# Performance work log

Measured on AMD Instinct MI355X. Metric: run time of the kernel, lower is better.

The kernel has to match this reference:

```python
import jax, jax.numpy as jnp
import numpy as np
import math

B, S, D = 4, 2048, 1024
N_HEADS = 16
D_FF = 4096
T_DIM = 256
KEEP_RATIO = 0.7
EPS = 1e-5


def _layernorm(x):
    mu = jnp.mean(x, axis=-1, keepdims=True)
    var = jnp.mean((x - mu) ** 2, axis=-1, keepdims=True)
    return (x - mu) * jax.lax.rsqrt(var + EPS)


def _ada_ln(x, cond, W, b):
    # cond: (B, T_DIM); W: (2D, T_DIM)
    p = jax.nn.silu(cond) @ W.T + b            # (B, 2D)
    gamma, beta = jnp.split(p, 2, axis=-1)
    return _layernorm(x) * (1.0 + gamma[:, None, :]) + beta[:, None, :]


def _mha(h, in_w, in_b, out_w, out_b):
    b, s, d = h.shape
    hd = d // N_HEADS
    qkv = h @ in_w.T + in_b                     # (b, s, 3d)
    q, k, v = jnp.split(qkv, 3, axis=-1)
    def heads(t):
        return t.reshape(b, s, N_HEADS, hd).transpose(0, 2, 1, 3)
    q, k, v = heads(q), heads(k), heads(v)
    scores = jnp.einsum('bhqd,bhkd->bhqk', q, k) / math.sqrt(hd)
    attn = jax.nn.softmax(scores, axis=-1)
    o = jnp.einsum('bhqk,bhkd->bhqd', attn, v)  # (b, h, s, hd)
    o = o.transpose(0, 2, 1, 3).reshape(b, s, d)
    return o @ out_w.T + out_b


def setup_inputs() -> dict:
    key = jax.random.key(0)
    ks = jax.random.split(key, 24)
    sc = 0.02
    return {
        'x': jax.random.normal(ks[0], (B, S, D), jnp.float32),
        't_emb': jax.random.normal(ks[1], (B, T_DIM), jnp.float32),
        'tr_w1': jax.random.normal(ks[2], (32, D), jnp.float32) * sc,
        'tr_b1': jnp.zeros((32,), jnp.float32),
        'tr_w2': jax.random.normal(ks[3], (1, 32), jnp.float32) * sc,
        'tr_b2': jnp.zeros((1,), jnp.float32),
        'ln1_w': jax.random.normal(ks[4], (2 * D, T_DIM), jnp.float32) * sc,
        'ln1_b': jnp.zeros((2 * D,), jnp.float32),
        'ln2_w': jax.random.normal(ks[5], (2 * D, T_DIM), jnp.float32) * sc,
        'ln2_b': jnp.zeros((2 * D,), jnp.float32),
        'in_proj_w': jax.random.normal(ks[6], (3 * D, D), jnp.float32) * sc,
        'in_proj_b': jnp.zeros((3 * D,), jnp.float32),
        'out_w': jax.random.normal(ks[7], (D, D), jnp.float32) * sc,
        'out_b': jnp.zeros((D,), jnp.float32),
        'ffn_w1': jax.random.normal(ks[8], (D_FF, D), jnp.float32) * sc,
        'ffn_b1': jnp.zeros((D_FF,), jnp.float32),
        'ffn_w2': jax.random.normal(ks[9], (D, D_FF), jnp.float32) * sc,
        'ffn_b2': jnp.zeros((D,), jnp.float32),
        # torch inits gates to zero; use small randn so the block is non-trivial
        'gate_attn': jax.random.normal(ks[10], (1, 1, D), jnp.float32) * sc,
        'gate_ffn': jax.random.normal(ks[11], (1, 1, D), jnp.float32) * sc,
    }


def reference(x, t_emb, tr_w1, tr_b1, tr_w2, tr_b2, ln1_w, ln1_b, ln2_w, ln2_b,
              in_proj_w, in_proj_b, out_w, out_b, ffn_w1, ffn_b1, ffn_w2, ffn_b2,
              gate_attn, gate_ffn):
    b, s, d = x.shape
    num_keep = max(int(s * KEEP_RATIO), 1)

    # token importance on detached x (stop_gradient mirrors x.detach())
    xd = jax.lax.stop_gradient(x)
    imp = jax.nn.silu(xd @ tr_w1.T + tr_b1) @ tr_w2.T + tr_b2  # (b, s, 1)
    imp = imp[..., 0]
    _, idx = jax.lax.top_k(imp, num_keep)
    idx = jnp.sort(idx, axis=-1)                               # (b, num_keep)

    x_sel = jnp.take_along_axis(x, idx[..., None], axis=1)     # (b, k, d)

    h = _ada_ln(x_sel, t_emb, ln1_w, ln1_b)
    h = _mha(h, in_proj_w, in_proj_b, out_w, out_b)
    x_sel = x_sel + gate_attn * h

    h = _ada_ln(x_sel, t_emb, ln2_w, ln2_b)
    h = jax.nn.gelu(h @ ffn_w1.T + ffn_b1, approximate=False) @ ffn_w2.T + ffn_b2
    x_sel = x_sel + gate_ffn * h

    batch_idx = jnp.arange(b)[:, None]
    return x.at[batch_idx, idx].set(x_sel)
```

## Files before the change

### kernel.cpp

```cpp
#include <hip/hip_runtime.h>
#include <hip/hip_bf16.h>
#include <cmath>
#include <cstdint>

typedef __bf16 bf16;
typedef __bf16 bf16x8 __attribute__((ext_vector_type(8)));
typedef __bf16 bf16x4 __attribute__((ext_vector_type(4)));
typedef float  f32x4  __attribute__((ext_vector_type(4)));

constexpr int B_   = 4;
constexpr int S_   = 2048;
constexpr int D_   = 1024;
constexpr int H_   = 16;
constexpr int DFF_ = 4096;
constexpr int TD_  = 256;
constexpr int KEEP = 1433;
constexpr int M_TOT = B_ * KEEP;
constexpr int MPAD  = 5760;
constexpr int QT64  = (KEEP + 63) / 64;
constexpr int NKV   = (KEEP + 63) / 64;
constexpr float EPS = 1e-5f;
constexpr float QSCALE = 0.18033688011112042f;

__device__ __forceinline__ f32x4 mfma16(bf16x8 a, bf16x8 b, f32x4 c) {
  return __builtin_amdgcn_mfma_f32_16x16x32_bf16(a, b, c, 0, 0, 0);
}

#define GLOAD_LDS(gp, lp)                                                     \
  __builtin_amdgcn_global_load_lds(                                           \
      (const __attribute__((address_space(1))) void*)(gp),                    \
      (__attribute__((address_space(3))) void*)(lp), 16, 0, 0)

__global__ __launch_bounds__(256) void k_impgemv(
    const float* __restrict__ x, const float* __restrict__ w1,
    double* __restrict__ hidden)
{
  const int lane = threadIdx.x & 63, w = threadIdx.x >> 6;
  const int tok0 = blockIdx.x * 16 + w * 4;
  const int u0 = blockIdx.y * 8;
  const float* xb = x + (size_t)tok0 * D_ + lane * 4;
  const float* wb = w1 + (size_t)u0 * D_ + lane * 4;
  double acc[4][8] = {};
#pragma unroll 2
  for (int c = 0; c < D_; c += 256) {
    float4 xv[4], wv[8];
#pragma unroll
    for (int i = 0; i < 4; ++i)
      xv[i] = *(const float4*)(xb + (size_t)i * D_ + c);
#pragma unroll
    for (int u = 0; u < 8; ++u)
      wv[u] = *(const float4*)(wb + (size_t)u * D_ + c);
#pragma unroll
    for (int i = 0; i < 4; ++i)
#pragma unroll
      for (int u = 0; u < 8; ++u) {
        acc[i][u] += (double)xv[i].x * (double)wv[u].x;
        acc[i][u] += (double)xv[i].y * (double)wv[u].y;
        acc[i][u] += (double)xv[i].z * (double)wv[u].z;
        acc[i][u] += (double)xv[i].w * (double)wv[u].w;
      }
  }
#pragma unroll
  for (int i = 0; i < 4; ++i)
#pragma unroll
    for (int u = 0; u < 8; ++u) {
      double s = acc[i][u];
      for (int o = 32; o > 0; o >>= 1) s += __shfl_xor(s, o);
      acc[i][u] = s;
    }
  if (lane == 0) {
#pragma unroll
    for (int i = 0; i < 4; ++i)
#pragma unroll
      for (int u = 0; u < 8; ++u)
        hidden[(size_t)(tok0 + i) * 32 + u0 + u] = acc[i][u];
  }
}

__global__ __launch_bounds__(256) void k_imptail(
    const double* __restrict__ hidden, const float* __restrict__ b1,
    const float* __restrict__ w2, const float* __restrict__ b2,
    double* __restrict__ imp)
{
  const int tok = blockIdx.x * 256 + threadIdx.x;
  const double* hp = hidden + (size_t)tok * 32;
  double r = 0.0;
#pragma unroll
  for (int u = 0; u < 32; ++u) {
    double s = hp[u] + (double)b1[u];
    double sv = s / (1.0 + exp(-s));
    r += sv * (double)w2[u];
  }
  imp[tok] = r + (double)b2[0];
}

__global__ __launch_bounds__(256) void k_rank(const double* __restrict__ imp,
                                              int* __restrict__ rank)
{
  const int b = blockIdx.x >> 5;
  const int seg = blockIdx.x & 31;
  __shared__ double vals[S_];
  const double* ib = imp + (size_t)b * S_;
  for (int i = threadIdx.x; i < S_ / 2; i += 256)
    ((double2*)vals)[i] = ((const double2*)ib)[i];
  __syncthreads();
  const int tl = threadIdx.x >> 2;
  const int part = threadIdx.x & 3;
  const int s = seg * 64 + tl;
  const double v = vals[s];
  int cnt = 0;
  for (int j = part * 512; j < (part + 1) * 512; ++j) {
    double u = vals[j];
    cnt += (u > v) || (u == v && j < s);
  }
  cnt += __shfl_xor(cnt, 1);
  cnt += __shfl_xor(cnt, 2);
  if (part == 0) rank[b * S_ + s] = cnt;
}

__global__ __launch_bounds__(256) void k_compact(const int* __restrict__ rank,
                                                 int* __restrict__ idx)
{
  const int b = blockIdx.x;
  __shared__ int wcnt[4];
  __shared__ int base_s;
  if (threadIdx.x == 0) base_s = 0;
  __syncthreads();
  const int t = threadIdx.x, lane = t & 63, w = t >> 6;
  for (int c = 0; c < S_ / 256; ++c) {
    const int s = c * 256 + t;
    const bool kept = rank[b * S_ + s] < KEEP;
    unsigned long long m = __ballot(kept);
    int piw = __popcll(m & ((1ull << lane) - 1ull));
    if (lane == 0) wcnt[w] = __popcll(m);
    __syncthreads();
    int off = base_s;
    for (int i = 0; i < w; ++i) off += wcnt[i];
    if (kept) idx[b * KEEP + off + piw] = s;
    __syncthreads();
    if (t == 0) base_s += wcnt[0] + wcnt[1] + wcnt[2] + wcnt[3];
    __syncthreads();
  }
}

__global__ __launch_bounds__(256) void k_condproj(
    const float* __restrict__ temb, const float* __restrict__ W,
    const float* __restrict__ bias, float* __restrict__ p)
{
  const int gw = (int)((blockIdx.x * 256 + threadIdx.x) >> 6);
  const int lane = threadIdx.x & 63;
  const int b = gw >> 11;
  const int row = gw & 2047;
  const float* te = temb + (size_t)b * TD_;
  const float* wr = W + (size_t)row * TD_;
  float acc = 0.f;
  for (int i = lane; i < TD_; i += 64) {
    float c = te[i];
    acc += (c / (1.f + __expf(-c))) * wr[i];
  }
  for (int o = 32; o > 0; o >>= 1) acc += __shfl_down(acc, o);
  if (lane == 0) p[(size_t)b * 2 * D_ + row] = acc + bias[row];
}

__global__ void k_f2b(const float* __restrict__ src, bf16* __restrict__ dst, int n4)
{
  int i = blockIdx.x * 256 + threadIdx.x;
  if (i < n4) {
    float4 v = ((const float4*)src)[i];
    bf16x4 o = {(bf16)v.x, (bf16)v.y, (bf16)v.z, (bf16)v.w};
    ((bf16x4*)dst)[i] = o;
  }
}

__global__ __launch_bounds__(256) void k_adaln(
    const float* __restrict__ xsrc, const int* __restrict__ idx,
    const float* __restrict__ p, bf16* __restrict__ hout)
{
  const int r = blockIdx.x, t = threadIdx.x;
  bf16* orow = hout + (size_t)r * D_;
  if (r >= M_TOT) {
    bf16x4 z = {(bf16)0.f, (bf16)0.f, (bf16)0.f, (bf16)0.f};
    ((bf16x4*)orow)[t] = z;
    return;
  }
  const int b = r / KEEP, j = r - b * KEEP;
  const int s = idx[b * KEEP + j];
  const float* xr = xsrc + ((size_t)(b * S_ + s)) * D_;
  float4 v = ((const float4*)xr)[t];
  __shared__ float red[8];
  float sum = v.x + v.y + v.z + v.w;
  for (int o = 32; o > 0; o >>= 1) sum += __shfl_down(sum, o);
  const int lane = t & 63, w = t >> 6;
  if (lane == 0) red[w] = sum;
  __syncthreads();
  const float mu = (red[0] + red[1] + red[2] + red[3]) * (1.f / D_);
  const float dx = v.x - mu, dy = v.y - mu, dz = v.z - mu, dw = v.w - mu;
  float vs = dx * dx + dy * dy + dz * dz + dw * dw;
  for (int o = 32; o > 0; o >>= 1) vs += __shfl_down(vs, o);
  if (lane == 0) red[4 + w] = vs;
  __syncthreads();
  const float rstd = rsqrtf((red[4] + red[5] + red[6] + red[7]) * (1.f / D_) + EPS);
  const float* gp = p + (size_t)b * 2 * D_;
  float4 g  = ((const float4*)gp)[t];
  float4 be = ((const float4*)(gp + D_))[t];
  bf16x4 o;
  o[0] = (bf16)(dx * rstd * (1.f + g.x) + be.x);
  o[1] = (bf16)(dy * rstd * (1.f + g.y) + be.y);
  o[2] = (bf16)(dz * rstd * (1.f + g.z) + be.z);
  o[3] = (bf16)(dw * rstd * (1.f + g.w) + be.w);
  ((bf16x4*)orow)[t] = o;
}

template <int BN, int MODE>
__global__ __launch_bounds__(256) void k_gemm(
    const bf16* __restrict__ A, const bf16* __restrict__ W,
    const float* __restrict__ bias, bf16* __restrict__ Cbf,
    const float* __restrict__ gate, const int* __restrict__ idx,
    float* __restrict__ resid, int N, int K, int gn)
{
  constexpr int WN = BN / 2;
  constexpr int NJ = WN / 16;
  __shared__ bf16 As[2][128 * 64];
  __shared__ bf16 Ws[2][BN * 64];
  const int t = threadIdx.x, lane = t & 63;
  const int w = t >> 6, wr = w >> 1, wc = w & 1;
  const int fr = lane & 15, fq = lane >> 4;

  const int nwg = gridDim.x, orig = blockIdx.x;
  const int q8 = nwg >> 3, r8 = nwg & 7;
  const int xc = orig & 7, pos = orig >> 3;
  const int wgid = (xc < r8 ? xc * (q8 + 1) : r8 * (q8 + 1) + (xc - r8) * q8) + pos;
  const int bm = wgid / gn, bn = wgid - bm * gn;

  const bf16* Ab = A + (size_t)bm * 128 * K;
  const bf16* Wb = W + (size_t)bn * BN * K;

  auto stage = [&](int buf, int kt) {
    const int ko = kt * 64;
#pragma unroll
    for (int it = 0; it < 4; ++it) {
      const int e = it * 256 + t;
      const int row = e >> 3, pc = e & 7;
      const int lc = pc ^ (row & 7);
      GLOAD_LDS(Ab + (size_t)row * K + ko + lc * 8, &As[buf][0] + e * 8);
    }
#pragma unroll
    for (int it = 0; it < BN / 32; ++it) {
      const int e = it * 256 + t;
      const int row = e >> 3, pc = e & 7;
      const int lc = pc ^ (row & 7);
      GLOAD_LDS(Wb + (size_t)row * K + ko + lc * 8, &Ws[buf][0] + e * 8);
    }
  };

  f32x4 acc[4][NJ] = {};
  stage(0, 0);
  const int nkt = K >> 6;
  int cur = 0;
  for (int kt = 0; kt < nkt; ++kt) {
    __syncthreads();
    if (kt + 1 < nkt) stage(cur ^ 1, kt + 1);
    const char* Al = (const char*)&As[cur][0];
    const char* Wl = (const char*)&Ws[cur][0];
#pragma unroll
    for (int kk = 0; kk < 2; ++kk) {
      bf16x8 af[4], wf[NJ];
#pragma unroll
      for (int i = 0; i < 4; ++i)
        af[i] = *(const bf16x8*)(Al + (wr * 64 + i * 16 + fr) * 128 +
                                 (((kk * 4 + fq) ^ (fr & 7)) << 4));
#pragma unroll
      for (int j = 0; j < NJ; ++j)
        wf[j] = *(const bf16x8*)(Wl + (wc * WN + j * 16 + fr) * 128 +
                                 (((kk * 4 + fq) ^ (fr & 7)) << 4));
#pragma unroll
      for (int i = 0; i < 4; ++i)
#pragma unroll
        for (int j = 0; j < NJ; ++j)
          acc[i][j] = mfma16(af[i], wf[j], acc[i][j]);
    }
    cur ^= 1;
  }

#pragma unroll
  for (int i = 0; i < 4; ++i) {
#pragma unroll
    for (int j = 0; j < NJ; ++j) {
#pragma unroll
      for (int r = 0; r < 4; ++r) {
        const int m = bm * 128 + wr * 64 + i * 16 + fq * 4 + r;
        const int n = bn * BN + wc * WN + j * 16 + fr;
        float v = acc[i][j][r] + bias[n];
        if (MODE == 0) {
          if (n < D_) v *= QSCALE;
          Cbf[(size_t)m * N + n] = (bf16)v;
        } else if (MODE == 1) {
          float gl = 0.5f * v * (1.f + erff(v * 0.70710678118654752f));
          Cbf[(size_t)m * N + n] = (bf16)gl;
        } else {
          if (m < M_TOT) {
            const int b = m / KEEP, jj = m - b * KEEP;
            const int s = idx[b * KEEP + jj];
            resid[((size_t)(b * S_ + s)) * D_ + n] += gate[n] * v;
          }
        }
      }
    }
  }
}

__global__ __launch_bounds__(256) void k_attn(const bf16* __restrict__ qkv,
                                              bf16* __restrict__ out)
{
  __shared__ bf16 Klds[2][64 * 64];
  __shared__ bf16 Vlds[2][64 * 64];

  const int t = threadIdx.x;
  const int lane = t & 63, w = t >> 6;
  const int fr = lane & 15, fq = lane >> 4;
  const int qt = blockIdx.x, h = blockIdx.y, b = blockIdx.z;
  const size_t rowbase = (size_t)b * KEEP;
  const size_t RS = 3 * D_;
  const bf16* kbase = qkv + rowbase * RS + D_ + h * 64;
  const bf16* vbase = qkv + rowbase * RS + 2 * D_ + h * 64;

  const int wq0 = qt * 64 + w * 16;
  const int qrow = min(wq0 + fr, KEEP - 1);
  const bf16* qp = qkv + (rowbase + qrow) * RS + h * 64 + fq * 8;
  const bf16x8 qf0 = *(const bf16x8*)qp;
  const bf16x8 qf1 = *(const bf16x8*)(qp + 32);

  f32x4 o[4] = {};
  float mrow = -INFINITY, lrow = 0.f;

  auto stage = [&](int buf, int kv) {
#pragma unroll
    for (int rnd = 0; rnd < 2; ++rnd) {
      const int p = rnd * 256 + t;
      {
        const int row = p >> 3, c8p = p & 7;
        const int c8 = c8p ^ ((row & 7) ^ (row >> 3));
        const int gr = min(kv + row, KEEP - 1);
        GLOAD_LDS(kbase + (size_t)gr * RS + c8 * 8, &Klds[buf][0] + p * 8);
      }
      {
        const int db = p >> 7, ksub = (p >> 3) & 15, jr = (p >> 1) & 3,
                  c8lo = p & 1;
        const int vrow = ksub * 4 + jr, vc8 = db * 2 + c8lo;
        const int gr = min(kv + vrow, KEEP - 1);
        GLOAD_LDS(vbase + (size_t)gr * RS + vc8 * 8, &Vlds[buf][0] + p * 8);
      }
    }
  };

  stage(0, 0);
  int cur = 0;

  const unsigned vbase_lds0 =
      (unsigned)(size_t)(__attribute__((address_space(3))) bf16*)&Vlds[0][0];
  const unsigned vbase_lds1 =
      (unsigned)(size_t)(__attribute__((address_space(3))) bf16*)&Vlds[1][0];

  for (int ti = 0; ti < NKV; ++ti) {
    const int kv = ti * 64;
    __syncthreads();
    if (ti + 1 < NKV) stage(cur ^ 1, kv + 64);

    const char* Kl = (const char*)&Klds[cur][0];

    f32x4 sc[4];
#pragma unroll
    for (int f = 0; f < 4; ++f) {
      const int row = ((f >> 1) << 5) + ((fr >> 2) << 3) + ((f & 1) << 1) +
                      (fr & 1) + (((fr >> 1) & 1) << 2);
      const int swz = (row & 7) ^ (row >> 3);
      const bf16x8 kf0 = *(const bf16x8*)(Kl + row * 128 + ((fq ^ swz) << 4));
      const bf16x8 kf1 =
          *(const bf16x8*)(Kl + row * 128 + (((fq ^ 4) ^ swz) << 4));
      f32x4 s = {0.f, 0.f, 0.f, 0.f};
      s = mfma16(kf0, qf0, s);
      s = mfma16(kf1, qf1, s);
      sc[f] = s;
    }

    if (ti == NKV - 1) {
#pragma unroll
      for (int f = 0; f < 4; ++f)
#pragma unroll
        for (int r = 0; r < 4; ++r) {
          const int kl = ((f >> 1) << 5) + (fq << 3) + ((f & 1) << 1) +
                         (r & 1) + ((r >> 1) << 2);
          if (kv + kl >= KEEP) sc[f][r] = -INFINITY;
        }
    }
    float mx = sc[0][0];
#pragma unroll
    for (int f = 0; f < 4; ++f)
#pragma unroll
      for (int r = 0; r < 4; ++r) mx = fmaxf(mx, sc[f][r]);
    mx = fmaxf(mx, __shfl_xor(mx, 16));
    mx = fmaxf(mx, __shfl_xor(mx, 32));
    const float mnew = fmaxf(mrow, mx);
    float ps = 0.f;
    bf16 pe[4][4];
#pragma unroll
    for (int f = 0; f < 4; ++f)
#pragma unroll
      for (int r = 0; r < 4; ++r) {
        const float pv = exp2f(sc[f][r] - mnew);
        ps += pv;
        pe[f][r] = (bf16)pv;
      }
    ps += __shfl_xor(ps, 16);
    ps += __shfl_xor(ps, 32);
    const float fac = exp2f(mrow - mnew);
    lrow = lrow * fac + ps;
    mrow = mnew;
#pragma unroll
    for (int db = 0; db < 4; ++db) {
      o[db][0] *= fac; o[db][1] *= fac; o[db][2] *= fac; o[db][3] *= fac;
    }

    const bf16x8 pb[2] = {
        {pe[0][0], pe[0][1], pe[1][0], pe[1][1],
         pe[0][2], pe[0][3], pe[1][2], pe[1][3]},
        {pe[2][0], pe[2][1], pe[3][0], pe[3][1],
         pe[2][2], pe[2][3], pe[3][2], pe[3][3]}};
    const unsigned vb =
        (cur ? vbase_lds1 : vbase_lds0) + ((unsigned)fq << 7);
#pragma unroll
    for (int c = 0; c < 2; ++c) {
      const unsigned addr = vb + c * 1024;
      bf16x4 t0, t1, t2, t3, t4, t5, t6, t7;
      asm volatile(
          "ds_read_b64_tr_b16 %0, %8 offset:0\n\t"
          "ds_read_b64_tr_b16 %1, %8 offset:128\n\t"
          "ds_read_b64_tr_b16 %2, %8 offset:2048\n\t"
          "ds_read_b64_tr_b16 %3, %8 offset:2176\n\t"
          "ds_read_b64_tr_b16 %4, %8 offset:4096\n\t"
          "ds_read_b64_tr_b16 %5, %8 offset:4224\n\t"
          "ds_read_b64_tr_b16 %6, %8 offset:6144\n\t"
          "ds_read_b64_tr_b16 %7, %8 offset:6272\n\t"
          "s_waitcnt lgkmcnt(0)"
          : "=&v"(t0), "=&v"(t1), "=&v"(t2), "=&v"(t3),
            "=&v"(t4), "=&v"(t5), "=&v"(t6), "=&v"(t7)
          : "v"(addr));
      const bf16x8 vf0 = __builtin_shufflevector(t0, t1, 0, 1, 2, 3, 4, 5, 6, 7);
      const bf16x8 vf1 = __builtin_shufflevector(t2, t3, 0, 1, 2, 3, 4, 5, 6, 7);
      const bf16x8 vf2 = __builtin_shufflevector(t4, t5, 0, 1, 2, 3, 4, 5, 6, 7);
      const bf16x8 vf3 = __builtin_shufflevector(t6, t7, 0, 1, 2, 3, 4, 5, 6, 7);
      o[0] = mfma16(vf0, pb[c], o[0]);
      o[1] = mfma16(vf1, pb[c], o[1]);
      o[2] = mfma16(vf2, pb[c], o[2]);
      o[3] = mfma16(vf3, pb[c], o[3]);
    }
    cur ^= 1;
  }

  const int q = wq0 + fr;
  if (q < KEEP) {
    const float inv = 1.f / lrow;
#pragma unroll
    for (int db = 0; db < 4; ++db) {
      bf16x4 wv = {(bf16)(o[db][0] * inv), (bf16)(o[db][1] * inv),
                   (bf16)(o[db][2] * inv), (bf16)(o[db][3] * inv)};
      *(bf16x4*)(out + (rowbase + q) * (size_t)D_ + h * 64 + db * 16 + fq * 4) =
          wv;
    }
  }
}

extern "C" void kernel_launch(void* const* d_in, const int* in_sizes, int n_in,
                              void* d_out, int out_size, void* d_ws, size_t ws_size,
                              hipStream_t stream)
{
  (void)in_sizes; (void)n_in; (void)out_size; (void)ws_size;
  const float* x      = (const float*)d_in[0];
  const float* t_emb  = (const float*)d_in[1];
  const float* tr_w1  = (const float*)d_in[2];
  const float* tr_b1  = (const float*)d_in[3];
  const float* tr_w2  = (const float*)d_in[4];
  const float* tr_b2  = (const float*)d_in[5];
  const float* ln1_w  = (const float*)d_in[6];
  const float* ln1_b  = (const float*)d_in[7];
  const float* ln2_w  = (const float*)d_in[8];
  const float* ln2_b  = (const float*)d_in[9];
  const float* in_w   = (const float*)d_in[10];
  const float* in_b   = (const float*)d_in[11];
  const float* out_w  = (const float*)d_in[12];
  const float* out_b  = (const float*)d_in[13];
  const float* f1_w   = (const float*)d_in[14];
  const float* f1_b   = (const float*)d_in[15];
  const float* f2_w   = (const float*)d_in[16];
  const float* f2_b   = (const float*)d_in[17];
  const float* gate_a = (const float*)d_in[18];
  const float* gate_f = (const float*)d_in[19];

  char* ws = (char*)d_ws;
  size_t off = 0;
  auto alloc = [&](size_t bytes) -> char* {
    char* p = ws + off;
    off = (off + bytes + 255) & ~(size_t)255;
    return p;
  };
  double* imp  = (double*)alloc((size_t)B_ * S_ * 8);
  double* hid  = (double*)alloc((size_t)B_ * S_ * 32 * 8);
  int* rank    = (int*)alloc((size_t)B_ * S_ * 4);
  int* idx     = (int*)alloc((size_t)B_ * KEEP * 4);
  float* p1    = (float*)alloc((size_t)B_ * 2 * D_ * 4);
  float* p2    = (float*)alloc((size_t)B_ * 2 * D_ * 4);
  bf16* w_in   = (bf16*)alloc((size_t)3 * D_ * D_ * 2);
  bf16* w_out  = (bf16*)alloc((size_t)D_ * D_ * 2);
  bf16* w_f1   = (bf16*)alloc((size_t)DFF_ * D_ * 2);
  bf16* w_f2   = (bf16*)alloc((size_t)D_ * DFF_ * 2);
  bf16* h_bf   = (bf16*)alloc((size_t)MPAD * D_ * 2);
  bf16* big    = (bf16*)alloc((size_t)MPAD * (3 * D_ + D_) * 2);
  bf16* qkv    = big;
  bf16* attn   = big + (size_t)MPAD * 3 * D_;
  bf16* ffn1   = big;

  hipMemcpyAsync(d_out, x, (size_t)B_ * S_ * D_ * 4, hipMemcpyDeviceToDevice, stream);

  k_impgemv<<<dim3(B_ * S_ / 16, 4), 256, 0, stream>>>(x, tr_w1, hid);
  k_imptail<<<B_ * S_ / 256, 256, 0, stream>>>(hid, tr_b1, tr_w2, tr_b2, imp);
  k_rank<<<B_ * 32, 256, 0, stream>>>(imp, rank);
  k_compact<<<B_, 256, 0, stream>>>(rank, idx);

  k_condproj<<<(B_ * 2 * D_) / 4, 256, 0, stream>>>(t_emb, ln1_w, ln1_b, p1);
  k_condproj<<<(B_ * 2 * D_) / 4, 256, 0, stream>>>(t_emb, ln2_w, ln2_b, p2);

  k_f2b<<<(3 * D_ * D_ / 4 + 255) / 256, 256, 0, stream>>>(in_w, w_in, 3 * D_ * D_ / 4);
  k_f2b<<<(D_ * D_ / 4 + 255) / 256, 256, 0, stream>>>(out_w, w_out, D_ * D_ / 4);
  k_f2b<<<(DFF_ * D_ / 4 + 255) / 256, 256, 0, stream>>>(f1_w, w_f1, DFF_ * D_ / 4);
  k_f2b<<<(DFF_ * D_ / 4 + 255) / 256, 256, 0, stream>>>(f2_w, w_f2, DFF_ * D_ / 4);

  k_adaln<<<MPAD, 256, 0, stream>>>(x, idx, p1, h_bf);
  k_gemm<128, 0><<<45 * 24, 256, 0, stream>>>(
      h_bf, w_in, in_b, qkv, nullptr, nullptr, nullptr, 3 * D_, D_, 24);
  k_attn<<<dim3(QT64, H_, B_), 256, 0, stream>>>(qkv, attn);
  k_gemm<64, 2><<<45 * 16, 256, 0, stream>>>(
      attn, w_out, out_b, nullptr, gate_a, idx, (float*)d_out, D_, D_, 16);
  k_adaln<<<MPAD, 256, 0, stream>>>((const float*)d_out, idx, p2, h_bf);
  k_gemm<128, 1><<<45 * 32, 256, 0, stream>>>(
      h_bf, w_f1, f1_b, ffn1, nullptr, nullptr, nullptr, DFF_, D_, 32);
  k_gemm<64, 2><<<45 * 16, 256, 0, stream>>>(
      ffn1, w_f2, f2_b, nullptr, gate_f, idx, (float*)d_out, D_, DFF_, 16);
}
```

Measured before the change: 457.8 us.

## Add 256x256 tile GEMM for QKV/FFN1 and streamline attention pipeline

Adds a new 512-thread GEMM kernel with 256x256 tiles, double-buffered direct-to-LDS loads, explicit vmcnt waits and an XCD-aware block remap. It is used for the QKV and FFN1 projections to raise operand reuse and cut global traffic per FLOP. M is padded to 5888 so that it divides by 256, and the other GEMM grids are adjusted to match. The attention kernel precomputes streaming K/V pointers, raises wave priority around the MFMAs, and skips the online-softmax rescale when the running max grows by less than a threshold. The larger tiles use much more LDS and registers per block, which lowers occupancy, and the lazy rescale carries a small numerical risk.

```diff
diff --git a/kernel.cpp b/kernel.cpp
--- a/kernel.cpp
+++ b/kernel.cpp
@@ -16,7 +16,7 @@
 constexpr int TD_  = 256;
 constexpr int KEEP = 1433;
 constexpr int M_TOT = B_ * KEEP;
-constexpr int MPAD  = 5760;
+constexpr int MPAD  = 5888;
 constexpr int QT64  = (KEEP + 63) / 64;
 constexpr int NKV   = (KEEP + 63) / 64;
 constexpr float EPS = 1e-5f;
@@ -30,6 +30,13 @@
   __builtin_amdgcn_global_load_lds(                                           \
       (const __attribute__((address_space(1))) void*)(gp),                    \
       (__attribute__((address_space(3))) void*)(lp), 16, 0, 0)
+
+#define FENCE_BARRIER()                                                       \
+  do {                                                                        \
+    __builtin_amdgcn_sched_barrier(0);                                        \
+    __builtin_amdgcn_s_barrier();                                             \
+    __builtin_amdgcn_sched_barrier(0);                                        \
+  } while (0)
 
 __global__ __launch_bounds__(256) void k_impgemv(
     const float* __restrict__ x, const float* __restrict__ w1,
@@ -309,6 +316,110 @@
   }
 }
 
+template <int MODE>
+__global__ __launch_bounds__(512) void k_gemm256(
+    const bf16* __restrict__ A, const bf16* __restrict__ W,
+    const float* __restrict__ bias, bf16* __restrict__ Cbf, int N, int K, int gn)
+{
+  __shared__ bf16 As[2][256 * 64];
+  __shared__ bf16 Ws[2][256 * 64];
+  const int t = threadIdx.x, lane = t & 63;
+  const int wid = t >> 6, wr = wid >> 2, wc = wid & 3;
+  const int fr = lane & 15, fq = lane >> 4;
+
+  const int nwg = gridDim.x, orig = blockIdx.x;
+  const int q8 = nwg >> 3, r8 = nwg & 7;
+  const int xc = orig & 7, pos = orig >> 3;
+  const int wgid = (xc < r8 ? xc * (q8 + 1) : r8 * (q8 + 1) + (xc - r8) * q8) + pos;
+  const int bm = wgid / gn, bn = wgid - bm * gn;
+
+  const bf16* Ab = A + (size_t)bm * 256 * K;
+  const bf16* Wb = W + (size_t)bn * 256 * K;
+
+  const bf16* pA[4];
+  const bf16* pW[4];
+#pragma unroll
+  for (int it = 0; it < 4; ++it) {
+    const int e = it * 512 + t;
+    const int row = e >> 3, pc = e & 7;
+    const int lc = pc ^ (row & 7);
+    pA[it] = Ab + (size_t)row * K + lc * 8;
+    pW[it] = Wb + (size_t)row * K + lc * 8;
+  }
+
+  auto stage = [&](int buf) {
+#pragma unroll
+    for (int it = 0; it < 4; ++it) {
+      const int e = it * 512 + t;
+      GLOAD_LDS(pA[it], &As[buf][0] + e * 8);
+      pA[it] += 64;
+    }
+#pragma unroll
+    for (int it = 0; it < 4; ++it) {
+      const int e = it * 512 + t;
+      GLOAD_LDS(pW[it], &Ws[buf][0] + e * 8);
+      pW[it] += 64;
+    }
+  };
+
+  f32x4 acc[8][4] = {};
+  stage(0);
+  stage(1);
+  const int nkt = K >> 6;
+
+  for (int kt = 0; kt < nkt; ++kt) {
+    if (kt < nkt - 1) {
+      asm volatile("s_waitcnt vmcnt(8)" ::: "memory");
+    } else {
+      asm volatile("s_waitcnt vmcnt(0)" ::: "memory");
+    }
+    FENCE_BARRIER();
+    const int c = kt & 1;
+    const char* Al = (const char*)&As[c][0];
+    const char* Wl = (const char*)&Ws[c][0];
+#pragma unroll
+    for (int kk = 0; kk < 2; ++kk) {
+      bf16x8 af[8], wf[4];
+      const int pcsel = ((kk * 4 + fq) ^ (fr & 7)) << 4;
+#pragma unroll
+      for (int i = 0; i < 8; ++i)
+        af[i] = *(const bf16x8*)(Al + (wr * 128 + i * 16 + fr) * 128 + pcsel);
+#pragma unroll
+      for (int j = 0; j < 4; ++j)
+        wf[j] = *(const bf16x8*)(Wl + (wc * 64 + j * 16 + fr) * 128 + pcsel);
+      __builtin_amdgcn_s_setprio(1);
+#pragma unroll
+      for (int i = 0; i < 8; ++i)
+#pragma unroll
+        for (int j = 0; j < 4; ++j)
+          acc[i][j] = mfma16(af[i], wf[j], acc[i][j]);
+      __builtin_amdgcn_s_setprio(0);
+    }
+    FENCE_BARRIER();
+    if (kt + 2 < nkt) stage(c);
+  }
+
+#pragma unroll
+  for (int i = 0; i < 8; ++i) {
+#pragma unroll
+    for (int j = 0; j < 4; ++j) {
+#pragma unroll
+      for (int r = 0; r < 4; ++r) {
+        const int m = bm * 256 + wr * 128 + i * 16 + fq * 4 + r;
+        const int n = bn * 256 + wc * 64 + j * 16 + fr;
+        float v = acc[i][j][r] + bias[n];
+        if (MODE == 0) {
+          if (n < D_) v *= QSCALE;
+          Cbf[(size_t)m * N + n] = (bf16)v;
+        } else {
+          float gl = 0.5f * v * (1.f + erff(v * 0.70710678118654752f));
+          Cbf[(size_t)m * N + n] = (bf16)gl;
+        }
+      }
+    }
+  }
+}
+
 __global__ __launch_bounds__(256) void k_attn(const bf16* __restrict__ qkv,
                                               bf16* __restrict__ out)
 {
@@ -333,27 +444,40 @@
   f32x4 o[4] = {};
   float mrow = -INFINITY, lrow = 0.f;
 
-  auto stage = [&](int buf, int kv) {
-#pragma unroll
-    for (int rnd = 0; rnd < 2; ++rnd) {
-      const int p = rnd * 256 + t;
-      {
-        const int row = p >> 3, c8p = p & 7;
-        const int c8 = c8p ^ ((row & 7) ^ (row >> 3));
-        const int gr = min(kv + row, KEEP - 1);
-        GLOAD_LDS(kbase + (size_t)gr * RS + c8 * 8, &Klds[buf][0] + p * 8);
-      }
-      {
-        const int db = p >> 7, ksub = (p >> 3) & 15, jr = (p >> 1) & 3,
-                  c8lo = p & 1;
-        const int vrow = ksub * 4 + jr, vc8 = db * 2 + c8lo;
-        const int gr = min(kv + vrow, KEEP - 1);
-        GLOAD_LDS(vbase + (size_t)gr * RS + vc8 * 8, &Vlds[buf][0] + p * 8);
-      }
-    }
+  const int p0 = t, p1 = 256 + t;
+  auto kaddr = [&](int p, int kv) {
+    const int row = p >> 3, c8p = p & 7;
+    const int c8 = c8p ^ ((row & 7) ^ (row >> 3));
+    const int gr = min(kv + row, KEEP - 1);
+    return kbase + (size_t)gr * RS + c8 * 8;
   };
-
-  stage(0, 0);
+  auto vaddr = [&](int p, int kv) {
+    const int db = p >> 7, ksub = (p >> 3) & 15, jr = (p >> 1) & 3,
+              c8lo = p & 1;
+    const int vrow = ksub * 4 + jr, vc8 = db * 2 + c8lo;
+    const int gr = min(kv + vrow, KEEP - 1);
+    return vbase + (size_t)gr * RS + vc8 * 8;
+  };
+  const bf16* kp0 = kaddr(p0, 0);
+  const bf16* kp1 = kaddr(p1, 0);
+  const bf16* vp0 = vaddr(p0, 0);
+  const bf16* vp1 = vaddr(p1, 0);
+
+  auto stage_fast = [&](int buf) {
+    GLOAD_LDS(kp0, &Klds[buf][0] + p0 * 8);
+    GLOAD_LDS(kp1, &Klds[buf][0] + p1 * 8);
+    GLOAD_LDS(vp0, &Vlds[buf][0] + p0 * 8);
+    GLOAD_LDS(vp1, &Vlds[buf][0] + p1 * 8);
+    kp0 += 64 * RS; kp1 += 64 * RS; vp0 += 64 * RS; vp1 += 64 * RS;
+  };
+  auto stage_last = [&](int buf, int kv) {
+    GLOAD_LDS(kaddr(p0, kv), &Klds[buf][0] + p0 * 8);
+    GLOAD_LDS(kaddr(p1, kv), &Klds[buf][0] + p1 * 8);
+    GLOAD_LDS(vaddr(p0, kv), &Vlds[buf][0] + p0 * 8);
+    GLOAD_LDS(vaddr(p1, kv), &Vlds[buf][0] + p1 * 8);
+  };
+
+  stage_fast(0);
   int cur = 0;
 
   const unsigned vbase_lds0 =
@@ -364,11 +488,13 @@
   for (int ti = 0; ti < NKV; ++ti) {
     const int kv = ti * 64;
     __syncthreads();
-    if (ti + 1 < NKV) stage(cur ^ 1, kv + 64);
+    if (ti < NKV - 2) stage_fast(cur ^ 1);
+    else if (ti == NKV - 2) stage_last(cur ^ 1, kv + 64);
 
     const char* Kl = (const char*)&Klds[cur][0];
 
     f32x4 sc[4];
+    __builtin_amdgcn_s_setprio(1);
 #pragma unroll
     for (int f = 0; f < 4; ++f) {
       const int row = ((f >> 1) << 5) + ((fr >> 2) << 3) + ((f & 1) << 1) +
@@ -382,6 +508,7 @@
       s = mfma16(kf1, qf1, s);
       sc[f] = s;
     }
+    __builtin_amdgcn_s_setprio(0);
 
     if (ti == NKV - 1) {
 #pragma unroll
@@ -400,7 +527,9 @@
       for (int r = 0; r < 4; ++r) mx = fmaxf(mx, sc[f][r]);
     mx = fmaxf(mx, __shfl_xor(mx, 16));
     mx = fmaxf(mx, __shfl_xor(mx, 32));
-    const float mnew = fmaxf(mrow, mx);
+
+    const bool noresc = __all(mx <= mrow + 8.f);
+    const float mnew = noresc ? mrow : fmaxf(mrow, mx);
     float ps = 0.f;
     bf16 pe[4][4];
 #pragma unroll
@@ -413,13 +542,16 @@
       }
     ps += __shfl_xor(ps, 16);
     ps += __shfl_xor(ps, 32);
-    const float fac = exp2f(mrow - mnew);
-    lrow = lrow * fac + ps;
-    mrow = mnew;
-#pragma unroll
-    for (int db = 0; db < 4; ++db) {
-      o[db][0] *= fac; o[db][1] *= fac; o[db][2] *= fac; o[db][3] *= fac;
-    }
+    if (!noresc) {
+      const float fac = exp2f(mrow - mnew);
+      lrow *= fac;
+#pragma unroll
+      for (int db = 0; db < 4; ++db) {
+        o[db][0] *= fac; o[db][1] *= fac; o[db][2] *= fac; o[db][3] *= fac;
+      }
+      mrow = mnew;
+    }
+    lrow += ps;
 
     const bf16x8 pb[2] = {
         {pe[0][0], pe[0][1], pe[1][0], pe[1][1],
@@ -449,10 +581,12 @@
       const bf16x8 vf1 = __builtin_shufflevector(t2, t3, 0, 1, 2, 3, 4, 5, 6, 7);
       const bf16x8 vf2 = __builtin_shufflevector(t4, t5, 0, 1, 2, 3, 4, 5, 6, 7);
       const bf16x8 vf3 = __builtin_shufflevector(t6, t7, 0, 1, 2, 3, 4, 5, 6, 7);
+      __builtin_amdgcn_s_setprio(1);
       o[0] = mfma16(vf0, pb[c], o[0]);
       o[1] = mfma16(vf1, pb[c], o[1]);
       o[2] = mfma16(vf2, pb[c], o[2]);
       o[3] = mfma16(vf3, pb[c], o[3]);
+      __builtin_amdgcn_s_setprio(0);
     }
     cur ^= 1;
   }
@@ -535,14 +669,14 @@
   k_f2b<<<(DFF_ * D_ / 4 + 255) / 256, 256, 0, stream>>>(f2_w, w_f2, DFF_ * D_ / 4);
 
   k_adaln<<<MPAD, 256, 0, stream>>>(x, idx, p1, h_bf);
-  k_gemm<128, 0><<<45 * 24, 256, 0, stream>>>(
-      h_bf, w_in, in_b, qkv, nullptr, nullptr, nullptr, 3 * D_, D_, 24);
+  k_gemm256<0><<<23 * 12, 512, 0, stream>>>(
+      h_bf, w_in, in_b, qkv, 3 * D_, D_, 12);
   k_attn<<<dim3(QT64, H_, B_), 256, 0, stream>>>(qkv, attn);
-  k_gemm<64, 2><<<45 * 16, 256, 0, stream>>>(
+  k_gemm<64, 2><<<46 * 16, 256, 0, stream>>>(
       attn, w_out, out_b, nullptr, gate_a, idx, (float*)d_out, D_, D_, 16);
   k_adaln<<<MPAD, 256, 0, stream>>>((const float*)d_out, idx, p2, h_bf);
-  k_gemm<128, 1><<<45 * 32, 256, 0, stream>>>(
-      h_bf, w_f1, f1_b, ffn1, nullptr, nullptr, nullptr, DFF_, D_, 32);
-  k_gemm<64, 2><<<45 * 16, 256, 0, stream>>>(
+  k_gemm256<1><<<23 * 16, 512, 0, stream>>>(
+      h_bf, w_f1, f1_b, ffn1, DFF_, D_, 16);
+  k_gemm<64, 2><<<46 * 16, 256, 0, stream>>>(
       ffn1, w_f2, f2_b, nullptr, gate_f, idx, (float*)d_out, D_, DFF_, 16);
 }
```

Result: slower. 487.6 us (+6.5%).
